# Kernel tuning notes

Measured on AMD Instinct MI355X. Metric: run time of the kernel, lower is better.

The kernel has to match this reference:

```python
import jax, jax.numpy as jnp
import numpy as np

# ---- static config (Phi-3-small layer 0, blocksparse branch) ----
HIDDEN = 4096
N_HEADS = 32
N_KV = 8
HEAD_DIM = HIDDEN // N_HEADS        # 128
Q_PER_KV = N_HEADS // N_KV          # 4
SEQ = 2048
ROPE_BASE = 1000000.0
POS_SCALE = 1.0
SM_SCALE = 1.0 / HEAD_DIM           # mup scaling, multiplier=1.0
BLOCK = 64
LOCAL_BLOCKS = 16
VERT_STRIDE = 8


def _blocksparse_mask(seq_len):
    """Dense [S,S] bool mask realizing the causal blocksparse pattern:
    query block i attends key block j iff j<=i and (i-j < LOCAL_BLOCKS or (j+1) % VERT_STRIDE == 0),
    with elementwise causality inside blocks. Built once in numpy (static)."""
    nb = seq_len // BLOCK
    qb = np.arange(nb)[:, None]
    kb = np.arange(nb)[None, :]
    bmask = (kb <= qb) & ((qb - kb < LOCAL_BLOCKS) | ((kb + 1) % VERT_STRIDE == 0))
    emask = np.kron(bmask, np.ones((BLOCK, BLOCK), dtype=bool))
    i = np.arange(seq_len)
    emask &= i[:, None] >= i[None, :]
    return jnp.asarray(emask)


def _rope(x, cos, sin):
    # x: [B, S, H, D]; cos/sin: [S, D]
    x1, x2 = jnp.split(x, 2, axis=-1)
    rot = jnp.concatenate([-x2, x1], axis=-1)
    return x * cos[None, :, None, :] + rot * sin[None, :, None, :]


def setup_inputs() -> dict:
    key = jax.random.key(0)
    k1, k2, k3, k4, k5 = jax.random.split(key, 5)
    qkv_out = (N_HEADS + 2 * N_KV) * HEAD_DIM  # 6144
    return {
        "hidden_states": jax.random.normal(k1, (1, SEQ, HIDDEN), dtype=jnp.float32),
        "w_qkv": jax.random.normal(k2, (qkv_out, HIDDEN), dtype=jnp.float32) * 0.02,
        "b_qkv": jnp.zeros((qkv_out,), dtype=jnp.float32),
        "w_dense": jax.random.normal(k3, (HIDDEN, HIDDEN), dtype=jnp.float32) * 0.02,
        "b_dense": jnp.zeros((HIDDEN,), dtype=jnp.float32),
    }


def reference(hidden_states, w_qkv, b_qkv, w_dense, b_dense):
    B, S, _ = hidden_states.shape
    # grouped QKV projection: [B,S,(H+2*KV)*D]
    qkv = jnp.einsum("bsh,oh->bso", hidden_states, w_qkv) + b_qkv
    # group layout: (group, q0..q3, k, v) per kv head
    qkv = qkv.reshape(B, S, N_KV, Q_PER_KV + 2, HEAD_DIM)
    q = qkv[:, :, :, :Q_PER_KV].reshape(B, S, N_HEADS, HEAD_DIM)
    k = qkv[:, :, :, Q_PER_KV]   # [B,S,KV,D]
    v = qkv[:, :, :, Q_PER_KV + 1]
    # rotary embeddings (HF rotate-half style)
    inv_freq = 1.0 / (ROPE_BASE ** (jnp.arange(0, HEAD_DIM, 2, dtype=jnp.float32) / HEAD_DIM))
    t = jnp.arange(S, dtype=jnp.float32) * POS_SCALE
    freqs = jnp.outer(t, inv_freq)               # [S, D/2]
    emb = jnp.concatenate([freqs, freqs], axis=-1)
    cos, sin = jnp.cos(emb), jnp.sin(emb)
    q = _rope(q, cos, sin)
    k = _rope(k, cos, sin)
    # GQA: replicate kv heads to match q heads
    k = jnp.repeat(k, Q_PER_KV, axis=2)          # [B,S,H,D]
    v = jnp.repeat(v, Q_PER_KV, axis=2)
    mask = _blocksparse_mask(S)                  # [S,S] bool
    scores = jnp.einsum("bqhd,bkhd->bhqk", q, k) * SM_SCALE
    scores = jnp.where(mask[None, None], scores, jnp.finfo(scores.dtype).min)
    probs = jax.nn.softmax(scores, axis=-1)
    ctx = jnp.einsum("bhqk,bkhd->bqhd", probs, v).reshape(B, S, HIDDEN)
    out = jnp.einsum("bsh,oh->bso", ctx, w_dense) + b_dense
    return out
```

## Files before the change

### kernel.cpp

```cpp
#include <hip/hip_runtime.h>
#include <hip/hip_bf16.h>

#define SEQ 2048
#define HIDDEN 4096
#define NH 32
#define NKV 8
#define HD 128
#define QKV_OUT 6144
#define QSCALE (0.0078125f * 1.4426950408889634f)

typedef __attribute__((ext_vector_type(8))) short bf16x8;
typedef __attribute__((ext_vector_type(4))) float f32x4;
typedef __attribute__((ext_vector_type(16))) float f32x16;

__device__ inline unsigned short f32_bf16(float f) {
  union { float f; unsigned int u; } v; v.f = f;
  unsigned int r = v.u + 0x7FFFu + ((v.u >> 16) & 1u);
  return (unsigned short)(r >> 16);
}
__device__ inline float bf16_f32(unsigned short u) {
  union { unsigned int u; float f; } v; v.u = (unsigned int)u << 16;
  return v.f;
}
__device__ inline unsigned int pk(float a, float b) {
  union { __hip_bfloat162 h; unsigned int u; } t;
  t.h = __float22bfloat162_rn(make_float2(a, b));
  return t.u;
}
__device__ inline void pswap(unsigned int &a, unsigned int &b) {
  auto r = __builtin_amdgcn_permlane32_swap((int)a, (int)b, false, false);
  a = (unsigned int)r[0]; b = (unsigned int)r[1];
}
__device__ inline float xmax32(float v) {
  int x = __builtin_bit_cast(int, v);
  auto r = __builtin_amdgcn_permlane32_swap(x, x, false, false);
  return fmaxf(__builtin_bit_cast(float, (int)r[0]), __builtin_bit_cast(float, (int)r[1]));
}
__device__ inline float xadd32(float v) {
  int x = __builtin_bit_cast(int, v);
  auto r = __builtin_amdgcn_permlane32_swap(x, x, false, false);
  return __builtin_bit_cast(float, (int)r[0]) + __builtin_bit_cast(float, (int)r[1]);
}

__global__ __launch_bounds__(256) void conv_bf16(const float* __restrict__ in,
                                                 unsigned short* __restrict__ out,
                                                 int n) {
  int i = (blockIdx.x * 256 + threadIdx.x) * 8;
  if (i + 8 > n) return;
  float4 a = *reinterpret_cast<const float4*>(in + i);
  float4 b = *reinterpret_cast<const float4*>(in + i + 4);
  unsigned short t[8];
  t[0] = f32_bf16(a.x); t[1] = f32_bf16(a.y); t[2] = f32_bf16(a.z); t[3] = f32_bf16(a.w);
  t[4] = f32_bf16(b.x); t[5] = f32_bf16(b.y); t[6] = f32_bf16(b.z); t[7] = f32_bf16(b.w);
  *reinterpret_cast<uint4*>(out + i) = *reinterpret_cast<uint4*>(t);
}

__global__ __launch_bounds__(256) void build_tab(float* __restrict__ ct,
                                                 float* __restrict__ st) {
  int idx = blockIdx.x * 256 + threadIdx.x;
  int s = idx >> 6, d = idx & 63;
  float inv = powf(1.0e6f, -(float)d * (1.0f / 64.0f));
  float f = (float)s * inv;
  ct[idx] = cosf(f);
  st[idx] = sinf(f);
}

template <int BM, int BN, int LA, int LB, int CR, int CC, bool OBF>
__global__ __launch_bounds__(512, 2) void gemm8(const unsigned short* __restrict__ A,
                                                const unsigned short* __restrict__ B,
                                                const float* __restrict__ bias,
                                                void* __restrict__ Cp,
                                                int M, int N, int K) {
  constexpr int MREP = BM / 32;
  constexpr int NREP = BN / 64;
  constexpr int MH = MREP / 2;
  constexpr int HALF = (BM + BN) * 64;
  constexpr int BUF = HALF * 2;
  constexpr int LP = LA + LB;
  __shared__ __align__(16) char Lds[BUF * 2];

  const int tid = threadIdx.x;
  const int wave = tid >> 6, lane = tid & 63;
  const int wr = wave >> 2, wc = wave & 3;
  const int lrow = lane & 15, lgrp = lane >> 4;

  const int ntx = N / BN;
  const int wg0 = blockIdx.x;
  const int xcd = wg0 & 7, w = wg0 >> 3;
  constexpr int CPB = 0;
  const int cpb = ntx / CC;
  const int band = xcd / cpb, colc = xcd % cpb;
  const int bmi = band * CR + w / CC;
  const int bni = colc * CC + w % CC;
  const int bm = bmi * BM, bn = bni * BN;

  const int srow = lane >> 2;
  const int scol = ((lane & 3) ^ ((lane >= 32) ? 2 : 0)) * 8;
  const unsigned short* gA = A + (size_t)(bm + wave * (BM / 8) + srow) * K + scol;
  const unsigned short* gB = B + (size_t)(bn + wave * (BN / 8) + srow) * K + scol;
  const int ldsAw = wave * (BM / 8) * 64;
  const int ldsBw = BM * 64 + wave * (BN / 8) * 64;

  auto stage = [&](int bufb, int h, int k0) {
#pragma unroll
    for (int i = 0; i < LA; ++i)
      __builtin_amdgcn_global_load_lds(
          (const __attribute__((address_space(1))) unsigned int*)(gA + (size_t)(i * 16) * K + k0 + h * 32),
          (__attribute__((address_space(3))) unsigned int*)(Lds + bufb + h * HALF + ldsAw + i * 1024),
          16, 0, 0);
#pragma unroll
    for (int i = 0; i < LB; ++i)
      __builtin_amdgcn_global_load_lds(
          (const __attribute__((address_space(1))) unsigned int*)(gB + (size_t)(i * 16) * K + k0 + h * 32),
          (__attribute__((address_space(3))) unsigned int*)(Lds + bufb + h * HALF + ldsBw + i * 1024),
          16, 0, 0);
  };

  const int flip = ((lrow >> 3) & 1) << 5;
  const int aoff = (wr * (BM / 2) + lrow) * 64 + ((lgrp * 16) ^ flip);
  const int boff = BM * 64 + (wc * (BN / 4) + lrow) * 64 + ((lgrp * 16) ^ flip);

  f32x4 acc[MREP][NREP] = {};

  auto phase = [&](int cur, int h) {
    const char* base = Lds + cur + h * HALF;
    bf16x8 af[MREP], bfr[NREP];
#pragma unroll
    for (int m = 0; m < MH; ++m)
      af[m] = *reinterpret_cast<const bf16x8*>(base + aoff + m * 1024);
#pragma unroll
    for (int n = 0; n < NREP; ++n)
      bfr[n] = *reinterpret_cast<const bf16x8*>(base + boff + n * 1024);
    asm volatile("s_waitcnt lgkmcnt(0)" ::: "memory");
    __builtin_amdgcn_sched_barrier(0);
    __builtin_amdgcn_s_setprio(1);
#pragma unroll
    for (int m = 0; m < MH; ++m)
#pragma unroll
      for (int n = 0; n < NREP; ++n)
        acc[m][n] = __builtin_amdgcn_mfma_f32_16x16x32_bf16(af[m], bfr[n], acc[m][n], 0, 0, 0);
    __builtin_amdgcn_s_setprio(0);
    __builtin_amdgcn_sched_barrier(0);
#pragma unroll
    for (int m = MH; m < MREP; ++m)
      af[m] = *reinterpret_cast<const bf16x8*>(base + aoff + m * 1024);
    __builtin_amdgcn_s_barrier();
    asm volatile("s_waitcnt lgkmcnt(0)" ::: "memory");
    __builtin_amdgcn_sched_barrier(0);
    __builtin_amdgcn_s_setprio(1);
#pragma unroll
    for (int m = MH; m < MREP; ++m)
#pragma unroll
      for (int n = 0; n < NREP; ++n)
        acc[m][n] = __builtin_amdgcn_mfma_f32_16x16x32_bf16(af[m], bfr[n], acc[m][n], 0, 0, 0);
    __builtin_amdgcn_s_setprio(0);
  };

  const int nt = K / 64;
  stage(0, 0, 0);
  stage(0, 1, 0);
  for (int t = 0; t < nt - 1; ++t) {
    const int cur = (t & 1) ? BUF : 0;
    const int nxt = cur ^ BUF;
    const int k1 = (t + 1) * 64;
#pragma unroll
    for (int h = 0; h < 2; ++h) {
      stage(nxt, h, k1);
      if constexpr (LP == 4) asm volatile("s_waitcnt vmcnt(8)" ::: "memory");
      else                   asm volatile("s_waitcnt vmcnt(6)" ::: "memory");
      __builtin_amdgcn_s_barrier();
      asm volatile("" ::: "memory");
      phase(cur, h);
    }
  }
  {
    const int cur = ((nt - 1) & 1) ? BUF : 0;
    if constexpr (LP == 4) asm volatile("s_waitcnt vmcnt(4)" ::: "memory");
    else                   asm volatile("s_waitcnt vmcnt(3)" ::: "memory");
    __builtin_amdgcn_s_barrier();
    asm volatile("" ::: "memory");
    phase(cur, 0);
    asm volatile("s_waitcnt vmcnt(0)" ::: "memory");
    __builtin_amdgcn_s_barrier();
    asm volatile("" ::: "memory");
    phase(cur, 1);
  }

#pragma unroll
  for (int n = 0; n < NREP; ++n) {
    int col = bn + wc * (BN / 4) + n * 16 + lrow;
    float bv = bias[col];
#pragma unroll
    for (int m = 0; m < MREP; ++m)
#pragma unroll
      for (int r = 0; r < 4; ++r) {
        int row = bm + wr * (BM / 2) + m * 16 + lgrp * 4 + r;
        if constexpr (OBF)
          ((unsigned short*)Cp)[(size_t)row * N + col] = f32_bf16(acc[m][n][r] + bv);
        else
          ((float*)Cp)[(size_t)row * N + col] = acc[m][n][r] + bv;
      }
  }
}

__global__ __launch_bounds__(256) void rope_split(const unsigned short* __restrict__ qkvb,
                                                  const float* __restrict__ ct,
                                                  const float* __restrict__ st,
                                                  unsigned short* __restrict__ Q,
                                                  unsigned short* __restrict__ Kh,
                                                  unsigned short* __restrict__ Vt) {
  int b = blockIdx.x;
  if (b < 5120) {
    int t = b * 256 + threadIdx.x;
    int d8 = (t & 15) * 8;
    int q = t >> 4;
    int s = q / 40;
    int slotg = q - s * 40;
    int g = slotg / 5, slot = slotg - g * 5;
    const unsigned short* base = qkvb + (size_t)s * QKV_OUT + g * 768 + slot * 128;
    bf16x8 x8 = *reinterpret_cast<const bf16x8*>(base + d8);
    bf16x8 r8 = *reinterpret_cast<const bf16x8*>(base + (d8 ^ 64));
    float4 c0 = *reinterpret_cast<const float4*>(ct + s * 64 + (d8 & 63));
    float4 c1 = *reinterpret_cast<const float4*>(ct + s * 64 + (d8 & 63) + 4);
    float4 s0 = *reinterpret_cast<const float4*>(st + s * 64 + (d8 & 63));
    float4 s1 = *reinterpret_cast<const float4*>(st + s * 64 + (d8 & 63) + 4);
    float cc[8] = {c0.x, c0.y, c0.z, c0.w, c1.x, c1.y, c1.z, c1.w};
    float ss[8] = {s0.x, s0.y, s0.z, s0.w, s1.x, s1.y, s1.z, s1.w};
    float sgn = (d8 < 64) ? -1.0f : 1.0f;
    float sc = (slot < 4) ? QSCALE : 1.0f;
    unsigned short o[8];
#pragma unroll
    for (int i = 0; i < 8; ++i) {
      float x = bf16_f32((unsigned short)x8[i]);
      float r = bf16_f32((unsigned short)r8[i]) * sgn;
      o[i] = f32_bf16((x * cc[i] + r * ss[i]) * sc);
    }
    unsigned short* dst = (slot < 4)
        ? Q + ((size_t)(g * 4 + slot) * SEQ + s) * HD + d8
        : Kh + ((size_t)g * SEQ + s) * HD + d8;
    *reinterpret_cast<uint4*>(dst) = *reinterpret_cast<uint4*>(o);
  } else {
    int t2 = (b - 5120) * 256 + threadIdx.x;
    int d = t2 & 127;
    int rest = t2 >> 7;
    int g = rest & 7;
    int s0 = (rest >> 3) * 8;
    const unsigned short* src = qkvb + (size_t)s0 * QKV_OUT + g * 768 + 640 + d;
    unsigned short o[8];
#pragma unroll
    for (int i = 0; i < 8; ++i) o[i] = src[(size_t)i * QKV_OUT];
    *reinterpret_cast<uint4*>(&Vt[((size_t)g * HD + d) * SEQ + s0]) =
        *reinterpret_cast<uint4*>(o);
  }
}

__device__ inline int nextj(int x, int qb) {
  if (x > qb) return -1;
  if (qb - x < 16) return x;
  int v = (x & ~7) + 7;
  int w = qb - 15;
  return v < w ? v : w;
}

__global__ __launch_bounds__(256, 2) void attn32(const unsigned short* __restrict__ Q,
                                                 const unsigned short* __restrict__ Kh,
                                                 const unsigned short* __restrict__ Vt,
                                                 unsigned short* __restrict__ ctx) {
  const int g = blockIdx.x;
  const int y = (int)gridDim.y - 1 - (int)blockIdx.y;
  const int qb = y >> 1, half = y & 1;
  const int Q0 = y * 32;
  const int tid = threadIdx.x;
  const int wave = tid >> 6;
  const int h = g * 4 + wave;
  const int lane = tid & 63;
  const int l31 = lane & 31, hi = lane >> 5;

  __shared__ __align__(16) char Lds[65536];

  auto stage = [&](int bufb, int j) {
#pragma unroll
    for (int i = 0; i < 4; ++i) {
      int row = i * 16 + (tid >> 4);
      const unsigned short* src =
          Kh + ((size_t)(g * SEQ + j * 64 + row)) * HD + ((tid & 15) ^ (row & 15)) * 8;
      __builtin_amdgcn_global_load_lds(
          (const __attribute__((address_space(1))) unsigned int*)src,
          (__attribute__((address_space(3))) unsigned int*)(Lds + bufb + i * 4096 + (tid >> 6) * 1024),
          16, 0, 0);
    }
#pragma unroll
    for (int i = 0; i < 4; ++i) {
      int row = i * 32 + (tid >> 3);
      const unsigned short* src =
          Vt + ((size_t)(g * HD + row)) * SEQ + j * 64 + ((tid & 7) ^ (row & 7)) * 8;
      __builtin_amdgcn_global_load_lds(
          (const __attribute__((address_space(1))) unsigned int*)src,
          (__attribute__((address_space(3))) unsigned int*)(Lds + bufb + 16384 + i * 4096 + (tid >> 6) * 1024),
          16, 0, 0);
    }
  };

  bf16x8 qf[8];
  const unsigned short* qbase = Q + ((size_t)h * SEQ + Q0 + l31) * HD;
#pragma unroll
  for (int kk = 0; kk < 8; ++kk)
    qf[kk] = *reinterpret_cast<const bf16x8*>(qbase + kk * 16 + hi * 8);

  f32x16 ot[4] = {};
  float mrow = -1e30f, lsum = 0.f;

  const int kswz = l31 & 15;
  const int vswz = l31 & 7;

  int j = nextj(0, qb);
  int cur = 0;
  stage(0, j);
  asm volatile("s_waitcnt vmcnt(0)" ::: "memory");
  __builtin_amdgcn_sched_barrier(0);
  __builtin_amdgcn_s_barrier();
  __builtin_amdgcn_sched_barrier(0);

  while (true) {
    const int jn = (j < qb) ? nextj(j + 1, qb) : -1;
    if (jn >= 0) stage(cur ^ 32768, jn);

    const char* kb = Lds + cur;
    const char* vb = Lds + cur + 16384;
    const bool diag = (j == qb);
    const bool short_blk = diag && (half == 0);

    f32x16 st[2] = {};
    __builtin_amdgcn_s_setprio(1);
#pragma unroll
    for (int kk = 0; kk < 8; ++kk) {
      bf16x8 k0 = *reinterpret_cast<const bf16x8*>(
          kb + (size_t)l31 * 256 + (((2 * kk + hi) ^ kswz) * 16));
      st[0] = __builtin_amdgcn_mfma_f32_32x32x16_bf16(k0, qf[kk], st[0], 0, 0, 0);
      if (!short_blk) {
        bf16x8 k1 = *reinterpret_cast<const bf16x8*>(
            kb + (size_t)(32 + l31) * 256 + (((2 * kk + hi) ^ kswz) * 16));
        st[1] = __builtin_amdgcn_mfma_f32_32x32x16_bf16(k1, qf[kk], st[1], 0, 0, 0);
      }
    }
    __builtin_amdgcn_s_setprio(0);

    if (diag) {
      int qrel = half * 32 + l31;
#pragma unroll
      for (int kt = 0; kt < 2; ++kt)
#pragma unroll
        for (int r = 0; r < 16; ++r) {
          int krel = kt * 32 + (r & 3) + 8 * (r >> 2) + 4 * hi;
          if (krel > qrel) st[kt][r] = -1e30f;
        }
    }

    float t16[16];
#pragma unroll
    for (int r = 0; r < 16; ++r) t16[r] = fmaxf(st[0][r], st[1][r]);
#pragma unroll
    for (int sft = 8; sft >= 1; sft >>= 1)
#pragma unroll
      for (int r = 0; r < sft; ++r) t16[r] = fmaxf(t16[r], t16[r + sft]);
    float vm = xmax32(t16[0]);

    if (!__all(vm - mrow <= 8.0f)) {
      float nm = fmaxf(mrow, vm);
      float corr = __builtin_amdgcn_exp2f(mrow - nm);
      lsum *= corr;
#pragma unroll
      for (int dt = 0; dt < 4; ++dt)
#pragma unroll
        for (int r = 0; r < 16; ++r) ot[dt][r] *= corr;
      mrow = nm;
    }

    float s4[4] = {0.f, 0.f, 0.f, 0.f};
#pragma unroll
    for (int kt = 0; kt < 2; ++kt)
#pragma unroll
      for (int r = 0; r < 16; ++r) {
        float p = __builtin_amdgcn_exp2f(st[kt][r] - mrow);
        st[kt][r] = p;
        s4[r & 3] += p;
      }
    lsum += xadd32((s4[0] + s4[1]) + (s4[2] + s4[3]));

    bf16x8 pb[4];
#pragma unroll
    for (int s = 0; s < 4; ++s) {
      int kt = s >> 1, g0 = (s & 1) * 2, g1 = g0 + 1;
      unsigned int a0 = pk(st[kt][4 * g0 + 0], st[kt][4 * g0 + 1]);
      unsigned int a1 = pk(st[kt][4 * g0 + 2], st[kt][4 * g0 + 3]);
      unsigned int b0 = pk(st[kt][4 * g1 + 0], st[kt][4 * g1 + 1]);
      unsigned int b1 = pk(st[kt][4 * g1 + 2], st[kt][4 * g1 + 3]);
      pswap(a0, b0);
      pswap(a1, b1);
      union { unsigned int u[4]; bf16x8 v; } t;
      t.u[0] = a0; t.u[1] = a1; t.u[2] = b0; t.u[3] = b1;
      pb[s] = t.v;
    }

    const int smax = short_blk ? 2 : 4;
    __builtin_amdgcn_s_setprio(1);
#pragma unroll
    for (int dt = 0; dt < 4; ++dt) {
      const char* vrow = vb + (size_t)(dt * 32 + l31) * 128;
#pragma unroll
      for (int s = 0; s < 4; ++s)
        if (s < smax)
          ot[dt] = __builtin_amdgcn_mfma_f32_32x32x16_bf16(
              *reinterpret_cast<const bf16x8*>(vrow + (((2 * s + hi) ^ vswz) * 16)),
              pb[s], ot[dt], 0, 0, 0);
    }
    __builtin_amdgcn_s_setprio(0);

    if (jn < 0) break;
    asm volatile("s_waitcnt vmcnt(0)" ::: "memory");
    __builtin_amdgcn_sched_barrier(0);
    __builtin_amdgcn_s_barrier();
    __builtin_amdgcn_sched_barrier(0);
    j = jn;
    cur ^= 32768;
  }

  __syncthreads();
  char* W = Lds + wave * 8192;
  float inv = 1.0f / lsum;
  const int swz = (l31 & 7) << 4;
#pragma unroll
  for (int dt = 0; dt < 4; ++dt)
#pragma unroll
    for (int gg = 0; gg < 4; ++gg) {
      unsigned int u0 = pk(ot[dt][4 * gg + 0] * inv, ot[dt][4 * gg + 1] * inv);
      unsigned int u1 = pk(ot[dt][4 * gg + 2] * inv, ot[dt][4 * gg + 3] * inv);
      int off = (dt * 64 + gg * 16 + hi * 8) ^ swz;
      *reinterpret_cast<uint2*>(W + l31 * 256 + off) = make_uint2(u0, u1);
    }
#pragma unroll
  for (int i = 0; i < 8; ++i) {
    int row = lane >> 1;
    int t = (lane & 1) * 8 + i;
    bf16x8 vv = *reinterpret_cast<const bf16x8*>(
        W + row * 256 + ((t * 16) ^ ((row & 7) << 4)));
    *reinterpret_cast<bf16x8*>(&ctx[(size_t)(Q0 + row) * HIDDEN + h * HD + t * 8]) = vv;
  }
}

extern "C" void kernel_launch(void* const* d_in, const int* in_sizes, int n_in,
                              void* d_out, int out_size, void* d_ws, size_t ws_size,
                              hipStream_t stream) {
  const float* hidden  = (const float*)d_in[0];
  const float* w_qkv   = (const float*)d_in[1];
  const float* b_qkv   = (const float*)d_in[2];
  const float* w_dense = (const float*)d_in[3];
  const float* b_dense = (const float*)d_in[4];
  float* out = (float*)d_out;

  char* p = (char*)d_ws;
  unsigned short* hid_bf  = (unsigned short*)p; p += (size_t)SEQ * HIDDEN * 2;
  unsigned short* wqkv_bf = (unsigned short*)p; p += (size_t)QKV_OUT * HIDDEN * 2;
  unsigned short* wd_bf   = (unsigned short*)p; p += (size_t)HIDDEN * HIDDEN * 2;
  unsigned short* qkvb    = (unsigned short*)p; p += (size_t)SEQ * QKV_OUT * 2;
  unsigned short* Qb      = (unsigned short*)p; p += (size_t)NH * SEQ * HD * 2;
  unsigned short* Kb      = (unsigned short*)p; p += (size_t)NKV * SEQ * HD * 2;
  unsigned short* Vt      = (unsigned short*)p; p += (size_t)NKV * HD * SEQ * 2;
  float* ct               = (float*)p;          p += (size_t)SEQ * 64 * 4;
  float* st               = (float*)p;          p += (size_t)SEQ * 64 * 4;
  unsigned short* ctx = hid_bf;

  conv_bf16<<<(SEQ * HIDDEN) / 2048, 256, 0, stream>>>(hidden, hid_bf, SEQ * HIDDEN);
  conv_bf16<<<(QKV_OUT * HIDDEN) / 2048, 256, 0, stream>>>(w_qkv, wqkv_bf, QKV_OUT * HIDDEN);
  conv_bf16<<<(HIDDEN * HIDDEN) / 2048, 256, 0, stream>>>(w_dense, wd_bf, HIDDEN * HIDDEN);
  build_tab<<<(SEQ * 64) / 256, 256, 0, stream>>>(ct, st);

  gemm8<256, 256, 2, 2, 4, 6, true>
      <<<dim3((SEQ / 256) * (QKV_OUT / 256)), 512, 0, stream>>>(
          hid_bf, wqkv_bf, b_qkv, qkvb, SEQ, QKV_OUT, HIDDEN);
  rope_split<<<5120 + 1024, 256, 0, stream>>>(qkvb, ct, st, Qb, Kb, Vt);
  attn32<<<dim3(NKV, SEQ / 32), 256, 0, stream>>>(Qb, Kb, Vt, ctx);
  gemm8<128, 256, 1, 2, 8, 4, false>
      <<<dim3((SEQ / 128) * (HIDDEN / 256)), 512, 0, stream>>>(
          ctx, wd_bf, b_dense, out, SEQ, HIDDEN, HIDDEN);
}
```

Before: 287.8 us.

## Restructure GEMM into four-quadrant pipeline with interleaved prefetch stages

```diff
diff --git a/kernel.cpp b/kernel.cpp
--- a/kernel.cpp
+++ b/kernel.cpp
@@ -65,18 +65,18 @@
   st[idx] = sinf(f);
 }
 
-template <int BM, int BN, int LA, int LB, int CR, int CC, bool OBF>
-__global__ __launch_bounds__(512, 2) void gemm8(const unsigned short* __restrict__ A,
+template <int BM, int CR, int CC, bool OBF>
+__global__ __launch_bounds__(512, 2) void gemm9(const unsigned short* __restrict__ A,
                                                 const unsigned short* __restrict__ B,
                                                 const float* __restrict__ bias,
                                                 void* __restrict__ Cp,
                                                 int M, int N, int K) {
-  constexpr int MREP = BM / 32;
-  constexpr int NREP = BN / 64;
-  constexpr int MH = MREP / 2;
-  constexpr int HALF = (BM + BN) * 64;
-  constexpr int BUF = HALF * 2;
-  constexpr int LP = LA + LB;
+  constexpr int BN = 256;
+  constexpr int MQ = BM / 64;
+  constexpr int La = BM / 128;
+  constexpr int Lb = 2;
+  constexpr int AH = BM * 64;
+  constexpr int BUF = 2 * AH + 32768;
   __shared__ __align__(16) char Lds[BUF * 2];
 
   const int tid = threadIdx.x;
@@ -87,118 +87,152 @@
   const int ntx = N / BN;
   const int wg0 = blockIdx.x;
   const int xcd = wg0 & 7, w = wg0 >> 3;
-  constexpr int CPB = 0;
   const int cpb = ntx / CC;
   const int band = xcd / cpb, colc = xcd % cpb;
-  const int bmi = band * CR + w / CC;
-  const int bni = colc * CC + w % CC;
-  const int bm = bmi * BM, bn = bni * BN;
-
-  const int srow = lane >> 2;
-  const int scol = ((lane & 3) ^ ((lane >= 32) ? 2 : 0)) * 8;
-  const unsigned short* gA = A + (size_t)(bm + wave * (BM / 8) + srow) * K + scol;
-  const unsigned short* gB = B + (size_t)(bn + wave * (BN / 8) + srow) * K + scol;
-  const int ldsAw = wave * (BM / 8) * 64;
-  const int ldsBw = BM * 64 + wave * (BN / 8) * 64;
-
-  auto stage = [&](int bufb, int h, int k0) {
-#pragma unroll
-    for (int i = 0; i < LA; ++i)
-      __builtin_amdgcn_global_load_lds(
-          (const __attribute__((address_space(1))) unsigned int*)(gA + (size_t)(i * 16) * K + k0 + h * 32),
-          (__attribute__((address_space(3))) unsigned int*)(Lds + bufb + h * HALF + ldsAw + i * 1024),
-          16, 0, 0);
-#pragma unroll
-    for (int i = 0; i < LB; ++i)
-      __builtin_amdgcn_global_load_lds(
-          (const __attribute__((address_space(1))) unsigned int*)(gB + (size_t)(i * 16) * K + k0 + h * 32),
-          (__attribute__((address_space(3))) unsigned int*)(Lds + bufb + h * HALF + ldsBw + i * 1024),
-          16, 0, 0);
+  const int bm = (band * CR + w / CC) * BM;
+  const int bn = (colc * CC + w % CC) * BN;
+
+  const int srow8 = lane >> 3;
+  const int scol = ((lane & 7) ^ srow8) * 8;
+  const unsigned short* gsrc[2 * La + 2 * Lb];
+  int ldsoff[2 * La + 2 * Lb];
+#pragma unroll
+  for (int u = 0; u < 2; ++u)
+#pragma unroll
+    for (int j = 0; j < La; ++j) {
+      int row = bm + u * (BM / 2) + (wave * La + j) * 8 + srow8;
+      gsrc[u * La + j] = A + (size_t)row * K + scol;
+      ldsoff[u * La + j] = u * AH + (wave * La + j) * 1024;
+    }
+#pragma unroll
+  for (int u = 0; u < 2; ++u)
+#pragma unroll
+    for (int j = 0; j < Lb; ++j) {
+      int row = bn + u * 128 + (wave * Lb + j) * 8 + srow8;
+      gsrc[2 * La + u * Lb + j] = B + (size_t)row * K + scol;
+      ldsoff[2 * La + u * Lb + j] = 2 * AH + u * 16384 + (wave * Lb + j) * 1024;
+    }
+
+  auto stage = [&](int bufb, int u, int k0) {
+    const int lo = (u < 2) ? u * La : 2 * La + (u - 2) * Lb;
+    const int nl = (u < 2) ? La : Lb;
+#pragma unroll
+    for (int j = 0; j < 4; ++j)
+      if (j < nl)
+        __builtin_amdgcn_global_load_lds(
+            (const __attribute__((address_space(1))) unsigned int*)(gsrc[lo + j] + k0),
+            (__attribute__((address_space(3))) unsigned int*)(Lds + bufb + ldsoff[lo + j]),
+            16, 0, 0);
   };
 
-  const int flip = ((lrow >> 3) & 1) << 5;
-  const int aoff = (wr * (BM / 2) + lrow) * 64 + ((lgrp * 16) ^ flip);
-  const int boff = BM * 64 + (wc * (BN / 4) + lrow) * 64 + ((lgrp * 16) ^ flip);
-
-  f32x4 acc[MREP][NREP] = {};
-
-  auto phase = [&](int cur, int h) {
-    const char* base = Lds + cur + h * HALF;
-    bf16x8 af[MREP], bfr[NREP];
-#pragma unroll
-    for (int m = 0; m < MH; ++m)
-      af[m] = *reinterpret_cast<const bf16x8*>(base + aoff + m * 1024);
-#pragma unroll
-    for (int n = 0; n < NREP; ++n)
-      bfr[n] = *reinterpret_cast<const bf16x8*>(base + boff + n * 1024);
-    asm volatile("s_waitcnt lgkmcnt(0)" ::: "memory");
-    __builtin_amdgcn_sched_barrier(0);
-    __builtin_amdgcn_s_setprio(1);
-#pragma unroll
-    for (int m = 0; m < MH; ++m)
-#pragma unroll
-      for (int n = 0; n < NREP; ++n)
-        acc[m][n] = __builtin_amdgcn_mfma_f32_16x16x32_bf16(af[m], bfr[n], acc[m][n], 0, 0, 0);
-    __builtin_amdgcn_s_setprio(0);
-    __builtin_amdgcn_sched_barrier(0);
-#pragma unroll
-    for (int m = MH; m < MREP; ++m)
-      af[m] = *reinterpret_cast<const bf16x8*>(base + aoff + m * 1024);
-    __builtin_amdgcn_s_barrier();
-    asm volatile("s_waitcnt lgkmcnt(0)" ::: "memory");
-    __builtin_amdgcn_sched_barrier(0);
-    __builtin_amdgcn_s_setprio(1);
-#pragma unroll
-    for (int m = MH; m < MREP; ++m)
-#pragma unroll
-      for (int n = 0; n < NREP; ++n)
-        acc[m][n] = __builtin_amdgcn_mfma_f32_16x16x32_bf16(af[m], bfr[n], acc[m][n], 0, 0, 0);
-    __builtin_amdgcn_s_setprio(0);
+  const int rsw = (lrow & 7) << 4;
+  auto aoff = [&](int mh, int m, int ks) {
+    int r = mh * (BM / 4) + m * 16 + lrow;
+    return wr * AH + r * 128 + ((ks * 64 + lgrp * 16) ^ rsw);
   };
+  auto boff = [&](int nh, int n, int ks) {
+    int r = (wc & 1) * 64 + nh * 32 + n * 16 + lrow;
+    return 2 * AH + (wc >> 1) * 16384 + r * 128 + ((ks * 64 + lgrp * 16) ^ rsw);
+  };
+
+  f32x4 acc[2 * MQ][4] = {};
+  bf16x8 af[MQ][2], bf0[2][2], bf1[2][2];
 
   const int nt = K / 64;
-  stage(0, 0, 0);
-  stage(0, 1, 0);
-  for (int t = 0; t < nt - 1; ++t) {
+#pragma unroll
+  for (int u = 0; u < 4; ++u) stage(0, u, 0);
+
+  for (int t = 0; t < nt; ++t) {
     const int cur = (t & 1) ? BUF : 0;
     const int nxt = cur ^ BUF;
+    const bool pf = (t + 1) < nt;
     const int k1 = (t + 1) * 64;
-#pragma unroll
-    for (int h = 0; h < 2; ++h) {
-      stage(nxt, h, k1);
-      if constexpr (LP == 4) asm volatile("s_waitcnt vmcnt(8)" ::: "memory");
-      else                   asm volatile("s_waitcnt vmcnt(6)" ::: "memory");
-      __builtin_amdgcn_s_barrier();
-      asm volatile("" ::: "memory");
-      phase(cur, h);
-    }
+    const char* base = Lds + cur;
+
+    if (pf) stage(nxt, 0, k1);
+    if (pf) { if constexpr (La == 2) asm volatile("s_waitcnt vmcnt(2)" ::: "memory");
+              else                   asm volatile("s_waitcnt vmcnt(1)" ::: "memory"); }
+    else      asm volatile("s_waitcnt vmcnt(0)" ::: "memory");
+    __builtin_amdgcn_sched_barrier(0);
+    __builtin_amdgcn_s_barrier();
+    __builtin_amdgcn_sched_barrier(0);
+#pragma unroll
+    for (int m = 0; m < MQ; ++m)
+#pragma unroll
+      for (int ks = 0; ks < 2; ++ks)
+        af[m][ks] = *reinterpret_cast<const bf16x8*>(base + aoff(0, m, ks));
+#pragma unroll
+    for (int n = 0; n < 2; ++n)
+#pragma unroll
+      for (int ks = 0; ks < 2; ++ks)
+        bf0[n][ks] = *reinterpret_cast<const bf16x8*>(base + boff(0, n, ks));
+    __builtin_amdgcn_s_setprio(1);
+#pragma unroll
+    for (int m = 0; m < MQ; ++m)
+#pragma unroll
+      for (int n = 0; n < 2; ++n)
+#pragma unroll
+        for (int ks = 0; ks < 2; ++ks)
+          acc[m][n] = __builtin_amdgcn_mfma_f32_16x16x32_bf16(af[m][ks], bf0[n][ks], acc[m][n], 0, 0, 0);
+    __builtin_amdgcn_s_setprio(0);
+
+    if (pf) stage(nxt, 1, k1);
+#pragma unroll
+    for (int n = 0; n < 2; ++n)
+#pragma unroll
+      for (int ks = 0; ks < 2; ++ks)
+        bf1[n][ks] = *reinterpret_cast<const bf16x8*>(base + boff(1, n, ks));
+    __builtin_amdgcn_s_setprio(1);
+#pragma unroll
+    for (int m = 0; m < MQ; ++m)
+#pragma unroll
+      for (int n = 0; n < 2; ++n)
+#pragma unroll
+        for (int ks = 0; ks < 2; ++ks)
+          acc[m][2 + n] = __builtin_amdgcn_mfma_f32_16x16x32_bf16(af[m][ks], bf1[n][ks], acc[m][2 + n], 0, 0, 0);
+    __builtin_amdgcn_s_setprio(0);
+
+    if (pf) stage(nxt, 2, k1);
+#pragma unroll
+    for (int m = 0; m < MQ; ++m)
+#pragma unroll
+      for (int ks = 0; ks < 2; ++ks)
+        af[m][ks] = *reinterpret_cast<const bf16x8*>(base + aoff(1, m, ks));
+    __builtin_amdgcn_s_setprio(1);
+#pragma unroll
+    for (int m = 0; m < MQ; ++m)
+#pragma unroll
+      for (int n = 0; n < 2; ++n)
+#pragma unroll
+        for (int ks = 0; ks < 2; ++ks)
+          acc[MQ + m][n] = __builtin_amdgcn_mfma_f32_16x16x32_bf16(af[m][ks], bf0[n][ks], acc[MQ + m][n], 0, 0, 0);
+    __builtin_amdgcn_s_setprio(0);
+
+    if (pf) stage(nxt, 3, k1);
+    __builtin_amdgcn_s_setprio(1);
+#pragma unroll
+    for (int m = 0; m < MQ; ++m)
+#pragma unroll
+      for (int n = 0; n < 2; ++n)
+#pragma unroll
+        for (int ks = 0; ks < 2; ++ks)
+          acc[MQ + m][2 + n] = __builtin_amdgcn_mfma_f32_16x16x32_bf16(af[m][ks], bf1[n][ks], acc[MQ + m][2 + n], 0, 0, 0);
+    __builtin_amdgcn_s_setprio(0);
   }
-  {
-    const int cur = ((nt - 1) & 1) ? BUF : 0;
-    if constexpr (LP == 4) asm volatile("s_waitcnt vmcnt(4)" ::: "memory");
-    else                   asm volatile("s_waitcnt vmcnt(3)" ::: "memory");
-    __builtin_amdgcn_s_barrier();
-    asm volatile("" ::: "memory");
-    phase(cur, 0);
-    asm volatile("s_waitcnt vmcnt(0)" ::: "memory");
-    __builtin_amdgcn_s_barrier();
-    asm volatile("" ::: "memory");
-    phase(cur, 1);
-  }
-
-#pragma unroll
-  for (int n = 0; n < NREP; ++n) {
-    int col = bn + wc * (BN / 4) + n * 16 + lrow;
+
+#pragma unroll
+  for (int ni = 0; ni < 4; ++ni) {
+    int col = bn + wc * 64 + ni * 16 + lrow;
     float bv = bias[col];
 #pragma unroll
-    for (int m = 0; m < MREP; ++m)
+    for (int mi = 0; mi < 2 * MQ; ++mi)
 #pragma unroll
       for (int r = 0; r < 4; ++r) {
-        int row = bm + wr * (BM / 2) + m * 16 + lgrp * 4 + r;
+        int row = bm + wr * (BM / 2) + mi * 16 + lgrp * 4 + r;
         if constexpr (OBF)
-          ((unsigned short*)Cp)[(size_t)row * N + col] = f32_bf16(acc[m][n][r] + bv);
+          ((unsigned short*)Cp)[(size_t)row * N + col] = f32_bf16(acc[mi][ni][r] + bv);
         else
-          ((float*)Cp)[(size_t)row * N + col] = acc[m][n][r] + bv;
+          ((float*)Cp)[(size_t)row * N + col] = acc[mi][ni][r] + bv;
       }
   }
 }
@@ -475,12 +509,12 @@
   conv_bf16<<<(HIDDEN * HIDDEN) / 2048, 256, 0, stream>>>(w_dense, wd_bf, HIDDEN * HIDDEN);
   build_tab<<<(SEQ * 64) / 256, 256, 0, stream>>>(ct, st);
 
-  gemm8<256, 256, 2, 2, 4, 6, true>
+  gemm9<256, 4, 6, true>
       <<<dim3((SEQ / 256) * (QKV_OUT / 256)), 512, 0, stream>>>(
           hid_bf, wqkv_bf, b_qkv, qkvb, SEQ, QKV_OUT, HIDDEN);
   rope_split<<<5120 + 1024, 256, 0, stream>>>(qkvb, ct, st, Qb, Kb, Vt);
   attn32<<<dim3(NKV, SEQ / 32), 256, 0, stream>>>(Qb, Kb, Vt, ctx);
-  gemm8<128, 256, 1, 2, 8, 4, false>
+  gemm9<128, 8, 4, false>
       <<<dim3((SEQ / 128) * (HIDDEN / 256)), 512, 0, stream>>>(
           ctx, wd_bf, b_dense, out, SEQ, HIDDEN, HIDDEN);
 }
```

Result: no change. 291.6 us (+1.3%).

## Replace GEMM with 4-stage BK=32 pipelined kernel using XOR-swizzled LDS

Applied to the files above, without the earlier changes.

```diff
diff --git a/kernel.cpp b/kernel.cpp
--- a/kernel.cpp
+++ b/kernel.cpp
@@ -65,19 +65,16 @@
   st[idx] = sinf(f);
 }
 
-template <int BM, int BN, int LA, int LB, int CR, int CC, bool OBF>
-__global__ __launch_bounds__(512, 2) void gemm8(const unsigned short* __restrict__ A,
+template <int CR, int CC, bool OBF>
+__global__ __launch_bounds__(512, 2) void gemmT(const unsigned short* __restrict__ A,
                                                 const unsigned short* __restrict__ B,
                                                 const float* __restrict__ bias,
                                                 void* __restrict__ Cp,
                                                 int M, int N, int K) {
-  constexpr int MREP = BM / 32;
-  constexpr int NREP = BN / 64;
-  constexpr int MH = MREP / 2;
-  constexpr int HALF = (BM + BN) * 64;
-  constexpr int BUF = HALF * 2;
-  constexpr int LP = LA + LB;
-  __shared__ __align__(16) char Lds[BUF * 2];
+  constexpr int BM = 128, BN = 256, BK = 32;
+  constexpr int ABYTES = BM * 64;
+  constexpr int BUFB = ABYTES + BN * 64;
+  __shared__ __align__(16) char Lds[BUFB * 4];
 
   const int tid = threadIdx.x;
   const int wave = tid >> 6, lane = tid & 63;
@@ -87,114 +84,82 @@
   const int ntx = N / BN;
   const int wg0 = blockIdx.x;
   const int xcd = wg0 & 7, w = wg0 >> 3;
-  constexpr int CPB = 0;
   const int cpb = ntx / CC;
   const int band = xcd / cpb, colc = xcd % cpb;
-  const int bmi = band * CR + w / CC;
-  const int bni = colc * CC + w % CC;
-  const int bm = bmi * BM, bn = bni * BN;
-
-  const int srow = lane >> 2;
-  const int scol = ((lane & 3) ^ ((lane >= 32) ? 2 : 0)) * 8;
-  const unsigned short* gA = A + (size_t)(bm + wave * (BM / 8) + srow) * K + scol;
-  const unsigned short* gB = B + (size_t)(bn + wave * (BN / 8) + srow) * K + scol;
-  const int ldsAw = wave * (BM / 8) * 64;
-  const int ldsBw = BM * 64 + wave * (BN / 8) * 64;
-
-  auto stage = [&](int bufb, int h, int k0) {
-#pragma unroll
-    for (int i = 0; i < LA; ++i)
-      __builtin_amdgcn_global_load_lds(
-          (const __attribute__((address_space(1))) unsigned int*)(gA + (size_t)(i * 16) * K + k0 + h * 32),
-          (__attribute__((address_space(3))) unsigned int*)(Lds + bufb + h * HALF + ldsAw + i * 1024),
-          16, 0, 0);
-#pragma unroll
-    for (int i = 0; i < LB; ++i)
-      __builtin_amdgcn_global_load_lds(
-          (const __attribute__((address_space(1))) unsigned int*)(gB + (size_t)(i * 16) * K + k0 + h * 32),
-          (__attribute__((address_space(3))) unsigned int*)(Lds + bufb + h * HALF + ldsBw + i * 1024),
-          16, 0, 0);
+  const int bm = (band * CR + w / CC) * BM;
+  const int bn = (colc * CC + w % CC) * BN;
+
+  const int r4 = lane >> 2;
+  const int csrc = ((lane & 3) ^ (r4 & 3) ^ ((r4 >> 2) & 3)) * 8;
+  const unsigned short* ga  = A + (size_t)(bm + wave * 16 + r4) * K + csrc;
+  const unsigned short* gb0 = B + (size_t)(bn + wave * 32 + r4) * K + csrc;
+  const unsigned short* gb1 = B + (size_t)(bn + wave * 32 + 16 + r4) * K + csrc;
+  const int la  = wave * 1024;
+  const int lb0 = ABYTES + wave * 2048;
+  const int lb1 = lb0 + 1024;
+
+  auto stage = [&](int t) {
+    const int bufb = (t & 3) * BUFB;
+    const int k0 = t * BK;
+    __builtin_amdgcn_global_load_lds(
+        (const __attribute__((address_space(1))) unsigned int*)(ga + k0),
+        (__attribute__((address_space(3))) unsigned int*)(Lds + bufb + la), 16, 0, 0);
+    __builtin_amdgcn_global_load_lds(
+        (const __attribute__((address_space(1))) unsigned int*)(gb0 + k0),
+        (__attribute__((address_space(3))) unsigned int*)(Lds + bufb + lb0), 16, 0, 0);
+    __builtin_amdgcn_global_load_lds(
+        (const __attribute__((address_space(1))) unsigned int*)(gb1 + k0),
+        (__attribute__((address_space(3))) unsigned int*)(Lds + bufb + lb1), 16, 0, 0);
   };
 
-  const int flip = ((lrow >> 3) & 1) << 5;
-  const int aoff = (wr * (BM / 2) + lrow) * 64 + ((lgrp * 16) ^ flip);
-  const int boff = BM * 64 + (wc * (BN / 4) + lrow) * 64 + ((lgrp * 16) ^ flip);
-
-  f32x4 acc[MREP][NREP] = {};
-
-  auto phase = [&](int cur, int h) {
-    const char* base = Lds + cur + h * HALF;
-    bf16x8 af[MREP], bfr[NREP];
-#pragma unroll
-    for (int m = 0; m < MH; ++m)
-      af[m] = *reinterpret_cast<const bf16x8*>(base + aoff + m * 1024);
-#pragma unroll
-    for (int n = 0; n < NREP; ++n)
-      bfr[n] = *reinterpret_cast<const bf16x8*>(base + boff + n * 1024);
-    asm volatile("s_waitcnt lgkmcnt(0)" ::: "memory");
+  const int csw = (lgrp ^ (lrow & 3) ^ ((lrow >> 2) & 3)) * 16;
+  const int abase = (wr * 64 + lrow) * 64 + csw;
+  const int bbase = ABYTES + (wc * 64 + lrow) * 64 + csw;
+
+  f32x4 acc[4][4] = {};
+  const int nt = K / BK;
+
+  stage(0);
+  stage(1);
+  for (int t = 0; t < nt; ++t) {
+    if (t + 2 < nt) {
+      stage(t + 2);
+      asm volatile("s_waitcnt vmcnt(6)" ::: "memory");
+    } else if (t + 1 < nt) {
+      asm volatile("s_waitcnt vmcnt(3)" ::: "memory");
+    } else {
+      asm volatile("s_waitcnt vmcnt(0)" ::: "memory");
+    }
     __builtin_amdgcn_sched_barrier(0);
+    __builtin_amdgcn_s_barrier();
+    __builtin_amdgcn_sched_barrier(0);
+
+    const char* base = Lds + (t & 3) * BUFB;
+    bf16x8 af[4], bf[4];
+#pragma unroll
+    for (int m = 0; m < 4; ++m)
+      af[m] = *reinterpret_cast<const bf16x8*>(base + abase + m * 1024);
+#pragma unroll
+    for (int n = 0; n < 4; ++n)
+      bf[n] = *reinterpret_cast<const bf16x8*>(base + bbase + n * 1024);
     __builtin_amdgcn_s_setprio(1);
 #pragma unroll
-    for (int m = 0; m < MH; ++m)
-#pragma unroll
-      for (int n = 0; n < NREP; ++n)
-        acc[m][n] = __builtin_amdgcn_mfma_f32_16x16x32_bf16(af[m], bfr[n], acc[m][n], 0, 0, 0);
+    for (int m = 0; m < 4; ++m)
+#pragma unroll
+      for (int n = 0; n < 4; ++n)
+        acc[m][n] = __builtin_amdgcn_mfma_f32_16x16x32_bf16(af[m], bf[n], acc[m][n], 0, 0, 0);
     __builtin_amdgcn_s_setprio(0);
-    __builtin_amdgcn_sched_barrier(0);
-#pragma unroll
-    for (int m = MH; m < MREP; ++m)
-      af[m] = *reinterpret_cast<const bf16x8*>(base + aoff + m * 1024);
-    __builtin_amdgcn_s_barrier();
-    asm volatile("s_waitcnt lgkmcnt(0)" ::: "memory");
-    __builtin_amdgcn_sched_barrier(0);
-    __builtin_amdgcn_s_setprio(1);
-#pragma unroll
-    for (int m = MH; m < MREP; ++m)
-#pragma unroll
-      for (int n = 0; n < NREP; ++n)
-        acc[m][n] = __builtin_amdgcn_mfma_f32_16x16x32_bf16(af[m], bfr[n], acc[m][n], 0, 0, 0);
-    __builtin_amdgcn_s_setprio(0);
-  };
-
-  const int nt = K / 64;
-  stage(0, 0, 0);
-  stage(0, 1, 0);
-  for (int t = 0; t < nt - 1; ++t) {
-    const int cur = (t & 1) ? BUF : 0;
-    const int nxt = cur ^ BUF;
-    const int k1 = (t + 1) * 64;
-#pragma unroll
-    for (int h = 0; h < 2; ++h) {
-      stage(nxt, h, k1);
-      if constexpr (LP == 4) asm volatile("s_waitcnt vmcnt(8)" ::: "memory");
-      else                   asm volatile("s_waitcnt vmcnt(6)" ::: "memory");
-      __builtin_amdgcn_s_barrier();
-      asm volatile("" ::: "memory");
-      phase(cur, h);
-    }
   }
-  {
-    const int cur = ((nt - 1) & 1) ? BUF : 0;
-    if constexpr (LP == 4) asm volatile("s_waitcnt vmcnt(4)" ::: "memory");
-    else                   asm volatile("s_waitcnt vmcnt(3)" ::: "memory");
-    __builtin_amdgcn_s_barrier();
-    asm volatile("" ::: "memory");
-    phase(cur, 0);
-    asm volatile("s_waitcnt vmcnt(0)" ::: "memory");
-    __builtin_amdgcn_s_barrier();
-    asm volatile("" ::: "memory");
-    phase(cur, 1);
-  }
-
-#pragma unroll
-  for (int n = 0; n < NREP; ++n) {
-    int col = bn + wc * (BN / 4) + n * 16 + lrow;
+
+#pragma unroll
+  for (int n = 0; n < 4; ++n) {
+    int col = bn + wc * 64 + n * 16 + lrow;
     float bv = bias[col];
 #pragma unroll
-    for (int m = 0; m < MREP; ++m)
+    for (int m = 0; m < 4; ++m)
 #pragma unroll
       for (int r = 0; r < 4; ++r) {
-        int row = bm + wr * (BM / 2) + m * 16 + lgrp * 4 + r;
+        int row = bm + wr * 64 + m * 16 + lgrp * 4 + r;
         if constexpr (OBF)
           ((unsigned short*)Cp)[(size_t)row * N + col] = f32_bf16(acc[m][n][r] + bv);
         else
@@ -475,12 +440,12 @@
   conv_bf16<<<(HIDDEN * HIDDEN) / 2048, 256, 0, stream>>>(w_dense, wd_bf, HIDDEN * HIDDEN);
   build_tab<<<(SEQ * 64) / 256, 256, 0, stream>>>(ct, st);
 
-  gemm8<256, 256, 2, 2, 4, 6, true>
-      <<<dim3((SEQ / 256) * (QKV_OUT / 256)), 512, 0, stream>>>(
+  gemmT<8, 6, true>
+      <<<dim3((SEQ / 128) * (QKV_OUT / 256)), 512, 0, stream>>>(
           hid_bf, wqkv_bf, b_qkv, qkvb, SEQ, QKV_OUT, HIDDEN);
   rope_split<<<5120 + 1024, 256, 0, stream>>>(qkvb, ct, st, Qb, Kb, Vt);
   attn32<<<dim3(NKV, SEQ / 32), 256, 0, stream>>>(Qb, Kb, Vt, ctx);
-  gemm8<128, 256, 1, 2, 8, 4, false>
+  gemmT<8, 4, false>
       <<<dim3((SEQ / 128) * (HIDDEN / 256)), 512, 0, stream>>>(
           ctx, wd_bf, b_dense, out, SEQ, HIDDEN, HIDDEN);
 }
```

Result: slower. 335.9 us (+16.7%).
